# Optimization experiments

Hardware: AMD Instinct MI355X
Metric: run time of the kernel (lower is better)

The kernel has to match this reference:

```python
import jax, jax.numpy as jnp
import numpy as np


def setup_inputs() -> dict:
    key = jax.random.key(0)
    ks = jax.random.split(key, 6)
    B, deep_C, shallow_C, H, W = 4, 256, 64, 64, 64
    qk_C = shallow_C // 4  # 16
    deep = jax.random.normal(ks[0], (B, deep_C, H, W), dtype=jnp.float32)
    shallow = jax.random.normal(ks[1], (B, shallow_C, H, W), dtype=jnp.float32)
    # 1x1 conv weights (out_ch, in_ch), fan-in scaled like torch conv init
    Wq = jax.random.normal(ks[2], (qk_C, shallow_C), dtype=jnp.float32) / np.sqrt(shallow_C)
    bq = jnp.zeros((qk_C,), dtype=jnp.float32)
    Wk = jax.random.normal(ks[3], (qk_C, shallow_C), dtype=jnp.float32) / np.sqrt(shallow_C)
    bk = jnp.zeros((qk_C,), dtype=jnp.float32)
    gamma = jnp.ones((1,), dtype=jnp.float32)
    return {"deep": deep, "shallow": shallow, "Wq": Wq, "bq": bq, "Wk": Wk, "bk": bk, "gamma": gamma}


def reference(deep, shallow, Wq, bq, Wk, bk, gamma):
    B, deep_C, H, W = deep.shape
    N = H * W
    # 1x1 convs == per-pixel linear maps
    q = jnp.einsum('oc,bchw->bohw', Wq, shallow) + bq[None, :, None, None]  # [B,qk_C,H,W]
    k = jnp.einsum('oc,bchw->bohw', Wk, shallow) + bk[None, :, None, None]
    qk_C = q.shape[1]
    q = q.reshape(B, qk_C, N)  # [B,qk_C,N]
    k = k.reshape(B, qk_C, N)
    # energy[b, i, j] = q_i . k_j  (NO 1/sqrt(d) scaling, faithful to original)
    energy = jnp.einsum('bci,bcj->bij', q, k)  # [B,N,N]
    attention = jax.nn.softmax(energy, axis=-1)  # [B,N,N]
    v = deep.reshape(B, deep_C, N)  # value taken directly from deep features
    # out = V @ attention^T : out[b,c,m] = sum_n v[b,c,n] * attention[b,m,n]
    out = jnp.einsum('bcn,bmn->bcm', v, attention)
    out = out.reshape(B, deep_C, H, W)
    return gamma * out + deep
```

## Files before the change

### kernel.cpp

```cpp
#include <hip/hip_runtime.h>
#include <hip/hip_bf16.h>
#include <stdint.h>

#define LOG2E 1.44269504088896340736f

typedef _Float16 f16x8  __attribute__((ext_vector_type(8)));
typedef __bf16   bf16x8 __attribute__((ext_vector_type(8)));
typedef float    f32x16 __attribute__((ext_vector_type(16)));

__device__ __forceinline__ uint32_t pack_f16_rn(float a, float b) {
    uint16_t ua = __builtin_bit_cast(uint16_t, (_Float16)a);
    uint16_t ub = __builtin_bit_cast(uint16_t, (_Float16)b);
    return (uint32_t)ua | ((uint32_t)ub << 16);
}
__device__ __forceinline__ uint32_t pack_bf2(float a, float b) {
    uint16_t ua = __builtin_bit_cast(uint16_t, (__bf16)a);
    uint16_t ub = __builtin_bit_cast(uint16_t, (__bf16)b);
    return (uint32_t)ua | ((uint32_t)ub << 16);
}

__global__ void __launch_bounds__(256) prepass(
    const float* __restrict__ deep, const float* __restrict__ shallow,
    const float* __restrict__ Wq, const float* __restrict__ bq,
    const float* __restrict__ Wk, const float* __restrict__ bk,
    uint16_t* __restrict__ Vb, uint16_t* __restrict__ Qb,
    uint16_t* __restrict__ Kb3) {
    __shared__ uint16_t tile[32 * 516];
    const int blk = blockIdx.x;
    if (blk < 64) {
        int gid = blk * 256 + threadIdx.x;
        int b = gid >> 12;
        int n = gid & 4095;
        const float* sp = shallow + (size_t)b * 64 * 4096 + n;
        float q[16], k[16];
#pragma unroll
        for (int o = 0; o < 16; ++o) { q[o] = bq[o]; k[o] = bk[o]; }
#pragma unroll 4
        for (int c = 0; c < 64; ++c) {
            float s = sp[(size_t)c * 4096];
#pragma unroll
            for (int o = 0; o < 16; ++o) {
                q[o] = fmaf(Wq[o * 64 + c], s, q[o]);
                k[o] = fmaf(Wk[o * 64 + c], s, k[o]);
            }
        }
        uint16_t* qr = Qb + (size_t)gid * 16;
        *(uint4*)(qr)     = make_uint4(pack_f16_rn(q[0]*LOG2E,  q[1]*LOG2E),
                                       pack_f16_rn(q[2]*LOG2E,  q[3]*LOG2E),
                                       pack_f16_rn(q[4]*LOG2E,  q[5]*LOG2E),
                                       pack_f16_rn(q[6]*LOG2E,  q[7]*LOG2E));
        *(uint4*)(qr + 8) = make_uint4(pack_f16_rn(q[8]*LOG2E,  q[9]*LOG2E),
                                       pack_f16_rn(q[10]*LOG2E, q[11]*LOG2E),
                                       pack_f16_rn(q[12]*LOG2E, q[13]*LOG2E),
                                       pack_f16_rn(q[14]*LOG2E, q[15]*LOG2E));
        uint16_t* kr = Kb3 + (size_t)(b * 128 + (n >> 5)) * 512 + (size_t)(n & 31) * 8;
        *(uint4*)(kr)       = make_uint4(pack_f16_rn(k[0],  k[1]),  pack_f16_rn(k[2],  k[3]),
                                         pack_f16_rn(k[4],  k[5]),  pack_f16_rn(k[6],  k[7]));
        *(uint4*)(kr + 256) = make_uint4(pack_f16_rn(k[8],  k[9]),  pack_f16_rn(k[10], k[11]),
                                         pack_f16_rn(k[12], k[13]), pack_f16_rn(k[14], k[15]));
    } else {
        const int vb_id = blk - 64;
        const int b  = vb_id >> 6;
        const int ct = (vb_id >> 3) & 7;
        const int kseg = vb_id & 7;
        const int tid = threadIdx.x;
        const int k4 = tid & 63;
        const int cb = tid >> 6;
        const size_t dbase = ((size_t)(b * 256 + ct * 32) * 4096) + kseg * 512;
#pragma unroll
        for (int p = 0; p < 16; ++p) {
            int c   = (p & 7) * 4 + cb;
            int key = (p >> 3) * 256 + k4 * 4;
            float4 f = *(const float4*)(deep + dbase + (size_t)c * 4096 + key);
            *(uint2*)&tile[c * 516 + key] =
                make_uint2(pack_bf2(f.x, f.y), pack_bf2(f.z, f.w));
        }
        __syncthreads();
        const int c   = tid & 31;
        const int h1  = (tid >> 5) & 1;
        const int kb0 = tid >> 6;
#pragma unroll
        for (int p2 = 0; p2 < 8; ++p2) {
            int kb = p2 * 4 + kb0;
            const uint16_t* t = &tile[c * 516 + kb * 16 + h1 * 8];
            uint2 lo = *(const uint2*)(t);
            uint2 hi = *(const uint2*)(t + 4);
            size_t u = (((size_t)((b * 8 + ct) * 256 + kseg * 32 + kb) * 2) + h1) * 32 + c;
            ((uint4*)Vb)[u] = make_uint4(lo.x, lo.y, hi.x, hi.y);
        }
    }
}

__global__ void __launch_bounds__(1024, 4) attn_main(
    const uint16_t* __restrict__ Qb, const uint16_t* __restrict__ Kb3,
    const uint16_t* __restrict__ Vb, const float* __restrict__ deep,
    const float* __restrict__ gamma, float* __restrict__ out) {
    const int lane = threadIdx.x & 63;
    const int w    = threadIdx.x >> 6;
    const int ks   = w & 7;
    const int sel  = w >> 3;
    const int col  = lane & 31;
    const int h1   = lane >> 5;

    const int bid = blockIdx.x;
    const int xcd = bid & 7;
    const int b   = xcd >> 1;
    const int qt  = ((bid >> 3) << 1) + (xcd & 1);
    const int n0q = qt * 64;

    __shared__ uint4 Pl[2][2][16][2][32];
    __shared__ float Lf[2][16][32];

    const uint16_t* qrow = Qb + ((size_t)(b * 4096 + n0q + sel * 32 + col)) * 16;
    uint4 ubq = *(const uint4*)(qrow + h1 * 8);

    const uint16_t* kbase = Kb3 + (size_t)b * 65536 + (size_t)ks * 512
                                + (size_t)lane * 8;
    const uint16_t* vlane = Vb + (size_t)(b * 8 + ks) * 131072
                               + (size_t)sel * 4096
                               + (size_t)h1 * 256 + (size_t)col * 8;

    f32x16 acc0 = {0,0,0,0,0,0,0,0,0,0,0,0,0,0,0,0};
    f32x16 acc1 = {0,0,0,0,0,0,0,0,0,0,0,0,0,0,0,0};
    float lacc = 0.0f;
    uint4 uk;

    auto qk_softmax = [&](int s) {
        const int pr = s & 1;
        f16x8 ak = __builtin_bit_cast(f16x8, uk);
        f16x8 bq = __builtin_bit_cast(f16x8, ubq);
        f32x16 e = {0,0,0,0,0,0,0,0,0,0,0,0,0,0,0,0};
        e = __builtin_amdgcn_mfma_f32_32x32x16_f16(ak, bq, e, 0, 0, 0);
        const int sn = (s < 15) ? s + 1 : s;
        uk = *(const uint4*)(kbase + (size_t)sn * 4096);
        float p[16];
#pragma unroll
        for (int r = 0; r < 16; ++r) p[r] = exp2f(e[r]);
        float t0 = (p[0] + p[1]) + (p[2] + p[3]);
        float t1 = (p[4] + p[5]) + (p[6] + p[7]);
        float t2 = (p[8] + p[9]) + (p[10] + p[11]);
        float t3 = (p[12] + p[13]) + (p[14] + p[15]);
        lacc += (t0 + t1) + (t2 + t3);
        uint32_t pk0 = pack_bf2(p[0],  p[1]),  pk1 = pack_bf2(p[2],  p[3]);
        uint32_t pk2 = pack_bf2(p[4],  p[5]),  pk3 = pack_bf2(p[6],  p[7]);
        uint32_t pk4 = pack_bf2(p[8],  p[9]),  pk5 = pack_bf2(p[10], p[11]);
        uint32_t pk6 = pack_bf2(p[12], p[13]), pk7 = pack_bf2(p[14], p[15]);
        ((uint2*)&Pl[pr][sel][2 * ks    ][0][col])[h1] = make_uint2(pk0, pk1);
        ((uint2*)&Pl[pr][sel][2 * ks    ][1][col])[h1] = make_uint2(pk2, pk3);
        ((uint2*)&Pl[pr][sel][2 * ks + 1][0][col])[h1] = make_uint2(pk4, pk5);
        ((uint2*)&Pl[pr][sel][2 * ks + 1][1][col])[h1] = make_uint2(pk6, pk7);
    };

#define LBAR()                                                      \
    {                                                               \
        asm volatile("s_waitcnt lgkmcnt(0)" ::: "memory");          \
        __builtin_amdgcn_s_barrier();                               \
    }

    uk = *(const uint4*)(kbase);
    qk_softmax(0);
    LBAR();

#pragma unroll 2
    for (int ss = 0; ss < 16; ++ss) {
        const int par = ss & 1;
        uint4 vr[8];
        const uint16_t* vss = vlane + (size_t)ss * 8192;
#pragma unroll
        for (int j = 0; j < 8; ++j) vr[j] = *(const uint4*)(vss + j * 512);

        if (ss < 15) qk_softmax(ss + 1);

        __builtin_amdgcn_s_setprio(1);
#pragma unroll
        for (int j = 0; j < 8; ++j) {
            const int f = sel * 8 + j;
            uint4 pb0 = Pl[par][0][f][h1][col];
            uint4 pb1 = Pl[par][1][f][h1][col];
            bf16x8 av = __builtin_bit_cast(bf16x8, vr[j]);
            acc0 = __builtin_amdgcn_mfma_f32_32x32x16_bf16(
                av, __builtin_bit_cast(bf16x8, pb0), acc0, 0, 0, 0);
            acc1 = __builtin_amdgcn_mfma_f32_32x32x16_bf16(
                av, __builtin_bit_cast(bf16x8, pb1), acc1, 0, 0, 0);
        }
        __builtin_amdgcn_s_setprio(0);
        LBAR();
    }

    Lf[sel][ks * 2 + h1][col] = lacc;
    float* Ex = (float*)&Pl[0][0][0][0][0];
    float* myEx = Ex + ((size_t)w * 64 + lane) * 16;
    if (w < 8) {
#pragma unroll
        for (int r = 0; r < 16; ++r) myEx[r] = acc1[r];
    } else {
#pragma unroll
        for (int r = 0; r < 16; ++r) myEx[r] = acc0[r];
    }
    LBAR();
    const float* pEx = Ex + ((size_t)(w ^ 8) * 64 + lane) * 16;
    float l = 0.0f;
#pragma unroll
    for (int j = 0; j < 16; ++j) l += Lf[sel][j][col];
    const float gr = gamma[0] / l;

    if (w < 8) {
#pragma unroll
        for (int r = 0; r < 16; ++r) {
            float a = acc0[r] + pEx[r];
            const int crow = (r & 3) + 8 * (r >> 2) + 4 * h1;
            size_t i0 = (size_t)(b * 256 + ks * 32 + crow) * 4096 + n0q + col;
            out[i0] = fmaf(gr, a, deep[i0]);
        }
    } else {
#pragma unroll
        for (int r = 0; r < 16; ++r) {
            float a = acc1[r] + pEx[r];
            const int crow = (r & 3) + 8 * (r >> 2) + 4 * h1;
            size_t i1 = (size_t)(b * 256 + ks * 32 + crow) * 4096 + n0q + 32 + col;
            out[i1] = fmaf(gr, a, deep[i1]);
        }
    }
#undef LBAR
}

extern "C" void kernel_launch(void* const* d_in, const int* in_sizes, int n_in,
                              void* d_out, int out_size, void* d_ws, size_t ws_size,
                              hipStream_t stream) {
    const float* deep    = (const float*)d_in[0];
    const float* shallow = (const float*)d_in[1];
    const float* Wq      = (const float*)d_in[2];
    const float* bq      = (const float*)d_in[3];
    const float* Wk      = (const float*)d_in[4];
    const float* bk      = (const float*)d_in[5];
    const float* gamma   = (const float*)d_in[6];
    float* out = (float*)d_out;

    uint16_t* Vb  = (uint16_t*)d_ws;
    uint16_t* Qb  = (uint16_t*)((char*)d_ws + (size_t)8 * 1024 * 1024);
    uint16_t* Kb3 = (uint16_t*)((char*)d_ws + (size_t)9 * 1024 * 1024);

    hipLaunchKernelGGL(prepass, dim3(320), dim3(256), 0, stream,
                       deep, shallow, Wq, bq, Wk, bk, Vb, Qb, Kb3);
    hipLaunchKernelGGL(attn_main, dim3(256), dim3(1024), 0, stream,
                       Qb, Kb3, Vb, deep, gamma, out);
}
```

Before: 72.71 us.

## Quad-buffer P tiles to halve barriers; split Q/K projection blocks

The attention kernel's P staging buffer in LDS grows from two to four slots. The QK/softmax stage now runs two steps ahead of the PV MFMA stage, and the loop issues one barrier per two key steps instead of one per step. Separately, the prepass gives the Q and K projections their own blocks, which doubles the projection block count and halves per-thread FMA work. The cost is twice the LDS for P tiles (about 128KB), more live registers from the deeper pipeline, and shallow-input reads done twice.

New measurement: 86.33 us. +18.7%, slower.

```diff
diff --git a/kernel.cpp b/kernel.cpp
--- a/kernel.cpp
+++ b/kernel.cpp
@@ -27,39 +27,42 @@
     uint16_t* __restrict__ Kb3) {
     __shared__ uint16_t tile[32 * 516];
     const int blk = blockIdx.x;
-    if (blk < 64) {
-        int gid = blk * 256 + threadIdx.x;
+    if (blk < 128) {
+        const bool doQ = (blk < 64);
+        int gid = (doQ ? blk : blk - 64) * 256 + threadIdx.x;
         int b = gid >> 12;
         int n = gid & 4095;
         const float* sp = shallow + (size_t)b * 64 * 4096 + n;
-        float q[16], k[16];
-#pragma unroll
-        for (int o = 0; o < 16; ++o) { q[o] = bq[o]; k[o] = bk[o]; }
+        const float* W  = doQ ? Wq : Wk;
+        const float* bi = doQ ? bq : bk;
+        float v[16];
+#pragma unroll
+        for (int o = 0; o < 16; ++o) v[o] = bi[o];
 #pragma unroll 4
         for (int c = 0; c < 64; ++c) {
             float s = sp[(size_t)c * 4096];
 #pragma unroll
-            for (int o = 0; o < 16; ++o) {
-                q[o] = fmaf(Wq[o * 64 + c], s, q[o]);
-                k[o] = fmaf(Wk[o * 64 + c], s, k[o]);
-            }
-        }
-        uint16_t* qr = Qb + (size_t)gid * 16;
-        *(uint4*)(qr)     = make_uint4(pack_f16_rn(q[0]*LOG2E,  q[1]*LOG2E),
-                                       pack_f16_rn(q[2]*LOG2E,  q[3]*LOG2E),
-                                       pack_f16_rn(q[4]*LOG2E,  q[5]*LOG2E),
-                                       pack_f16_rn(q[6]*LOG2E,  q[7]*LOG2E));
-        *(uint4*)(qr + 8) = make_uint4(pack_f16_rn(q[8]*LOG2E,  q[9]*LOG2E),
-                                       pack_f16_rn(q[10]*LOG2E, q[11]*LOG2E),
-                                       pack_f16_rn(q[12]*LOG2E, q[13]*LOG2E),
-                                       pack_f16_rn(q[14]*LOG2E, q[15]*LOG2E));
-        uint16_t* kr = Kb3 + (size_t)(b * 128 + (n >> 5)) * 512 + (size_t)(n & 31) * 8;
-        *(uint4*)(kr)       = make_uint4(pack_f16_rn(k[0],  k[1]),  pack_f16_rn(k[2],  k[3]),
-                                         pack_f16_rn(k[4],  k[5]),  pack_f16_rn(k[6],  k[7]));
-        *(uint4*)(kr + 256) = make_uint4(pack_f16_rn(k[8],  k[9]),  pack_f16_rn(k[10], k[11]),
-                                         pack_f16_rn(k[12], k[13]), pack_f16_rn(k[14], k[15]));
+            for (int o = 0; o < 16; ++o) v[o] = fmaf(W[o * 64 + c], s, v[o]);
+        }
+        if (doQ) {
+            uint16_t* qr = Qb + (size_t)gid * 16;
+            *(uint4*)(qr)     = make_uint4(pack_f16_rn(v[0]*LOG2E,  v[1]*LOG2E),
+                                           pack_f16_rn(v[2]*LOG2E,  v[3]*LOG2E),
+                                           pack_f16_rn(v[4]*LOG2E,  v[5]*LOG2E),
+                                           pack_f16_rn(v[6]*LOG2E,  v[7]*LOG2E));
+            *(uint4*)(qr + 8) = make_uint4(pack_f16_rn(v[8]*LOG2E,  v[9]*LOG2E),
+                                           pack_f16_rn(v[10]*LOG2E, v[11]*LOG2E),
+                                           pack_f16_rn(v[12]*LOG2E, v[13]*LOG2E),
+                                           pack_f16_rn(v[14]*LOG2E, v[15]*LOG2E));
+        } else {
+            uint16_t* kr = Kb3 + (size_t)(b * 128 + (n >> 5)) * 512 + (size_t)(n & 31) * 8;
+            *(uint4*)(kr)       = make_uint4(pack_f16_rn(v[0],  v[1]),  pack_f16_rn(v[2],  v[3]),
+                                             pack_f16_rn(v[4],  v[5]),  pack_f16_rn(v[6],  v[7]));
+            *(uint4*)(kr + 256) = make_uint4(pack_f16_rn(v[8],  v[9]),  pack_f16_rn(v[10], v[11]),
+                                             pack_f16_rn(v[12], v[13]), pack_f16_rn(v[14], v[15]));
+        }
     } else {
-        const int vb_id = blk - 64;
+        const int vb_id = blk - 128;
         const int b  = vb_id >> 6;
         const int ct = (vb_id >> 3) & 7;
         const int kseg = vb_id & 7;
@@ -108,7 +111,7 @@
     const int qt  = ((bid >> 3) << 1) + (xcd & 1);
     const int n0q = qt * 64;
 
-    __shared__ uint4 Pl[2][2][16][2][32];
+    __shared__ uint4 Pl[4][2][16][2][32];
     __shared__ float Lf[2][16][32];
 
     const uint16_t* qrow = Qb + ((size_t)(b * 4096 + n0q + sel * 32 + col)) * 16;
@@ -126,7 +129,7 @@
     uint4 uk;
 
     auto qk_softmax = [&](int s) {
-        const int pr = s & 1;
+        const int pr = s & 3;
         f16x8 ak = __builtin_bit_cast(f16x8, uk);
         f16x8 bq = __builtin_bit_cast(f16x8, ubq);
         f32x16 e = {0,0,0,0,0,0,0,0,0,0,0,0,0,0,0,0};
@@ -156,34 +159,43 @@
         asm volatile("s_waitcnt lgkmcnt(0)" ::: "memory");          \
         __builtin_amdgcn_s_barrier();                               \
     }
+#define PVSTEP(ss, vr)                                              \
+    {                                                               \
+        const int bk_ = (ss) & 3;                                   \
+        __builtin_amdgcn_s_setprio(1);                              \
+        _Pragma("unroll")                                           \
+        for (int j = 0; j < 8; ++j) {                               \
+            const int f = sel * 8 + j;                              \
+            uint4 pb0 = Pl[bk_][0][f][h1][col];                     \
+            uint4 pb1 = Pl[bk_][1][f][h1][col];                     \
+            bf16x8 av = __builtin_bit_cast(bf16x8, vr[j]);          \
+            acc0 = __builtin_amdgcn_mfma_f32_32x32x16_bf16(         \
+                av, __builtin_bit_cast(bf16x8, pb0), acc0, 0, 0, 0);\
+            acc1 = __builtin_amdgcn_mfma_f32_32x32x16_bf16(         \
+                av, __builtin_bit_cast(bf16x8, pb1), acc1, 0, 0, 0);\
+        }                                                           \
+        __builtin_amdgcn_s_setprio(0);                              \
+    }
 
     uk = *(const uint4*)(kbase);
     qk_softmax(0);
+    qk_softmax(1);
     LBAR();
 
-#pragma unroll 2
-    for (int ss = 0; ss < 16; ++ss) {
-        const int par = ss & 1;
+    for (int s2 = 0; s2 < 8; ++s2) {
+        const int ss0 = s2 * 2;
+        const int ss1 = ss0 + 1;
         uint4 vr[8];
-        const uint16_t* vss = vlane + (size_t)ss * 8192;
-#pragma unroll
-        for (int j = 0; j < 8; ++j) vr[j] = *(const uint4*)(vss + j * 512);
-
-        if (ss < 15) qk_softmax(ss + 1);
-
-        __builtin_amdgcn_s_setprio(1);
-#pragma unroll
-        for (int j = 0; j < 8; ++j) {
-            const int f = sel * 8 + j;
-            uint4 pb0 = Pl[par][0][f][h1][col];
-            uint4 pb1 = Pl[par][1][f][h1][col];
-            bf16x8 av = __builtin_bit_cast(bf16x8, vr[j]);
-            acc0 = __builtin_amdgcn_mfma_f32_32x32x16_bf16(
-                av, __builtin_bit_cast(bf16x8, pb0), acc0, 0, 0, 0);
-            acc1 = __builtin_amdgcn_mfma_f32_32x32x16_bf16(
-                av, __builtin_bit_cast(bf16x8, pb1), acc1, 0, 0, 0);
-        }
-        __builtin_amdgcn_s_setprio(0);
+        const uint16_t* vss0 = vlane + (size_t)ss0 * 8192;
+#pragma unroll
+        for (int j = 0; j < 8; ++j) vr[j] = *(const uint4*)(vss0 + j * 512);
+        if (ss0 + 2 < 16) qk_softmax(ss0 + 2);
+        PVSTEP(ss0, vr);
+        const uint16_t* vss1 = vlane + (size_t)ss1 * 8192;
+#pragma unroll
+        for (int j = 0; j < 8; ++j) vr[j] = *(const uint4*)(vss1 + j * 512);
+        if (ss0 + 3 < 16) qk_softmax(ss0 + 3);
+        PVSTEP(ss1, vr);
         LBAR();
     }
 
@@ -221,6 +233,7 @@
             out[i1] = fmaf(gr, a, deep[i1]);
         }
     }
+#undef PVSTEP
 #undef LBAR
 }
 
@@ -240,7 +253,7 @@
     uint16_t* Qb  = (uint16_t*)((char*)d_ws + (size_t)8 * 1024 * 1024);
     uint16_t* Kb3 = (uint16_t*)((char*)d_ws + (size_t)9 * 1024 * 1024);
 
-    hipLaunchKernelGGL(prepass, dim3(320), dim3(256), 0, stream,
+    hipLaunchKernelGGL(prepass, dim3(384), dim3(256), 0, stream,
                        deep, shallow, Wq, bq, Wk, bk, Vb, Qb, Kb3);
     hipLaunchKernelGGL(attn_main, dim3(256), dim3(1024), 0, stream,
                        Qb, Kb3, Vb, deep, gamma, out);
```
